# Kernel optimization log

Measured on AMD Instinct MI355X. Metric: run time of the kernel, lower is better.

The kernel has to match this reference:

```python
import jax, jax.numpy as jnp
import numpy as np

D = 512      # d_model
H = 8        # nhead
HD = D // H  # head dim
L = 8        # axis-0 length (torch seq dim, batch_first=False)
S = 128      # axis-1 length (torch batch dim; relation-tensor axis)
NL = 3       # encoder layers
EPS = 1e-5


def setup_inputs() -> dict:
    key = jax.random.key(0)
    ks = jax.random.split(key, 16)
    w = lambda k, shape: jax.random.normal(k, shape, jnp.float32) * 0.02
    return {
        "x": jax.random.normal(ks[0], (L, S, D), jnp.float32),
        # stacked per-layer transformer params (leading dim = NL)
        "attn_in_w": w(ks[1], (NL, 3 * D, D)), "attn_in_b": jnp.zeros((NL, 3 * D), jnp.float32),
        "attn_out_w": w(ks[2], (NL, D, D)),    "attn_out_b": jnp.zeros((NL, D), jnp.float32),
        "ln1_w": jnp.ones((NL, D), jnp.float32), "ln1_b": jnp.zeros((NL, D), jnp.float32),
        "ln2_w": jnp.ones((NL, D), jnp.float32), "ln2_b": jnp.zeros((NL, D), jnp.float32),
        "ff1_w": w(ks[3], (NL, 4 * D, D)), "ff1_b": jnp.zeros((NL, 4 * D), jnp.float32),
        "ff2_w": w(ks[4], (NL, D, 4 * D)), "ff2_b": jnp.zeros((NL, D), jnp.float32),
        "fln_w": jnp.ones((D,), jnp.float32), "fln_b": jnp.zeros((D,), jnp.float32),
        # 4 projection MLPs stacked: 0=sub, 1=obj, 2=verb_sub, 3=verb_obj
        "mlp_w0": w(ks[5], (4, D, D)), "mlp_b0": jnp.zeros((4, D), jnp.float32),
        "mlp_w1": w(ks[6], (4, D, D)), "mlp_b1": jnp.zeros((4, D), jnp.float32),
        "mlp_w2": w(ks[7], (4, D, D)), "mlp_b2": jnp.zeros((4, D), jnp.float32),
    }


def _ln(x, w, b):
    m = jnp.mean(x, axis=-1, keepdims=True)
    v = jnp.mean(jnp.square(x - m), axis=-1, keepdims=True)
    return (x - m) * jax.lax.rsqrt(v + EPS) * w + b


def _mha(x, in_w, in_b, out_w, out_b):
    # x: (L, B, D); attention over axis 0 (torch batch_first=False semantics)
    l, b, _ = x.shape
    qkv = x @ in_w.T + in_b                      # (L, B, 3D)
    q, k, v = jnp.split(qkv, 3, axis=-1)
    q = q.reshape(l, b, H, HD)
    k = k.reshape(l, b, H, HD)
    v = v.reshape(l, b, H, HD)
    scores = jnp.einsum("lbhd,mbhd->bhlm", q, k) / jnp.sqrt(jnp.float32(HD))
    attn = jax.nn.softmax(scores, axis=-1)
    o = jnp.einsum("bhlm,mbhd->lbhd", attn, v).reshape(l, b, D)
    return o @ out_w.T + out_b


def _mlp(x, w0, b0, w1, b1, w2, b2):
    h = jax.nn.relu(x @ w0.T + b0)
    h = jax.nn.relu(h @ w1.T + b1)
    return h @ w2.T + b2


def _forward(x, attn_in_w, attn_in_b, attn_out_w, attn_out_b,
             ln1_w, ln1_b, ln2_w, ln2_b, ff1_w, ff1_b, ff2_w, ff2_b,
             fln_w, fln_b, mlp_w0, mlp_b0, mlp_w1, mlp_b1, mlp_w2, mlp_b2):
    # TransformerEncoder (post-norm, relu, no dropout at eval)
    h = x
    for i in range(NL):
        h = _ln(h + _mha(h, attn_in_w[i], attn_in_b[i], attn_out_w[i], attn_out_b[i]),
                ln1_w[i], ln1_b[i])
        ff = jax.nn.relu(h @ ff1_w[i].T + ff1_b[i]) @ ff2_w[i].T + ff2_b[i]
        h = _ln(h + ff, ln2_w[i], ln2_b[i])
    h = _ln(h, fln_w, fln_b)  # final encoder norm

    sub = _mlp(h, mlp_w0[0], mlp_b0[0], mlp_w1[0], mlp_b1[0], mlp_w2[0], mlp_b2[0])
    obj = _mlp(h, mlp_w0[1], mlp_b0[1], mlp_w1[1], mlp_b1[1], mlp_w2[1], mlp_b2[1])
    vsub = _mlp(h, mlp_w0[2], mlp_b0[2], mlp_w1[2], mlp_b1[2], mlp_w2[2], mlp_b2[2])
    vobj = _mlp(h, mlp_w0[3], mlp_b0[3], mlp_w1[3], mlp_b1[3], mlp_w2[3], mlp_b2[3])

    # sub.unsqueeze(1) * vsub.unsqueeze(2): (B0, S, S, D)
    sub4 = sub[:, None, :, :] * vsub[:, :, None, :]
    obj4 = obj[:, None, :, :] * vobj[:, :, None, :]
    # p_x = sub4 @ obj4.transpose(-2, -1): (B0, S, S, S)
    return jnp.einsum("bijd,bikd->bijk", sub4, obj4)


def reference(x, attn_in_w, attn_in_b, attn_out_w, attn_out_b,
              ln1_w, ln1_b, ln2_w, ln2_b, ff1_w, ff1_b, ff2_w, ff2_b,
              fln_w, fln_b, mlp_w0, mlp_b0, mlp_w1, mlp_b1, mlp_w2, mlp_b2):
    return _forward(x, attn_in_w, attn_in_b, attn_out_w, attn_out_b,
                    ln1_w, ln1_b, ln2_w, ln2_b, ff1_w, ff1_b, ff2_w, ff2_b,
                    fln_w, fln_b, mlp_w0, mlp_b0, mlp_w1, mlp_b1, mlp_w2, mlp_b2)
```

## Files before the change

### kernel.cpp

```cpp
#include <hip/hip_runtime.h>

#define DEV __device__ __forceinline__

typedef __attribute__((ext_vector_type(8))) short bf16x8;
typedef __attribute__((ext_vector_type(8))) unsigned short u16x8;
typedef __attribute__((ext_vector_type(4))) float f32x4;

DEV unsigned short f2bf(float f) {
  unsigned int u = __float_as_uint(f);
  u += 0x7FFFu + ((u >> 16) & 1u);
  return (unsigned short)(u >> 16);
}
DEV float bf2f(unsigned short h) { return __uint_as_float(((unsigned int)h) << 16); }

DEV int swz(int row, int byteoff) { return row * 128 + (byteoff ^ ((row & 7) << 4)); }

__global__ void cvt_kernel(const float* __restrict__ src, unsigned short* __restrict__ dst,
                           float* __restrict__ dstf, int n) {
  long i = ((long)blockIdx.x * blockDim.x + threadIdx.x) * 8;
  long stride = (long)gridDim.x * blockDim.x * 8;
  for (; i < n; i += stride) {
    f32x4 a = *(const f32x4*)(src + i);
    f32x4 b = *(const f32x4*)(src + i + 4);
    u16x8 o;
    o[0] = f2bf(a[0]); o[1] = f2bf(a[1]); o[2] = f2bf(a[2]); o[3] = f2bf(a[3]);
    o[4] = f2bf(b[0]); o[5] = f2bf(b[1]); o[6] = f2bf(b[2]); o[7] = f2bf(b[3]);
    *(u16x8*)(dst + i) = o;
    if (dstf) { *(f32x4*)(dstf + i) = a; *(f32x4*)(dstf + i + 4) = b; }
  }
}

template <int ACT, int WF32, int WBF>
__global__ __launch_bounds__(256) void gemm_kernel(
    const unsigned short* __restrict__ X, const unsigned short* __restrict__ Wt,
    const float* __restrict__ bias, float* Yf, unsigned short* Ybf,
    int M, int N, int K, long xbs, long wbs, long bbs, long ybs) {
  __shared__ __align__(16) unsigned short As[64 * 64];
  __shared__ __align__(16) unsigned short Bs[64 * 64];
  const int t = threadIdx.x;
  const int bn = blockIdx.x, bm = blockIdx.y, bz = blockIdx.z;
  const unsigned short* Xp = X + (long)bz * xbs;
  const unsigned short* Wp = Wt + (long)bz * wbs;
  const float* bp = bias + (long)bz * bbs;

  const int lane = t & 63, wv = t >> 6;
  const int wr = wv >> 1, wc = wv & 1;
  f32x4 acc[2][2] = {};

  const int r = t >> 2;
  const int q = t & 3;
  const long xrow = (long)(bm * 64 + r) * K;
  const long wrow = (long)(bn * 64 + r) * K;
  char* Asb = (char*)As;
  char* Bsb = (char*)Bs;

  for (int kt = 0; kt < K; kt += 64) {
    const unsigned short* ga = Xp + xrow + kt + q * 16;
    const unsigned short* gb = Wp + wrow + kt + q * 16;
    u16x8 a0 = *(const u16x8*)ga;
    u16x8 a1 = *(const u16x8*)(ga + 8);
    u16x8 b0 = *(const u16x8*)gb;
    u16x8 b1 = *(const u16x8*)(gb + 8);
    *(u16x8*)(Asb + swz(r, q * 32)) = a0;
    *(u16x8*)(Asb + swz(r, q * 32 + 16)) = a1;
    *(u16x8*)(Bsb + swz(r, q * 32)) = b0;
    *(u16x8*)(Bsb + swz(r, q * 32 + 16)) = b1;
    __syncthreads();
#pragma unroll
    for (int kk = 0; kk < 2; ++kk) {
      const int kb = kk * 64 + ((lane >> 4) << 4);
      bf16x8 af[2], bfr[2];
#pragma unroll
      for (int mi = 0; mi < 2; ++mi)
        af[mi] = *(const bf16x8*)(Asb + swz(wr * 32 + mi * 16 + (lane & 15), kb));
#pragma unroll
      for (int ni = 0; ni < 2; ++ni)
        bfr[ni] = *(const bf16x8*)(Bsb + swz(wc * 32 + ni * 16 + (lane & 15), kb));
#pragma unroll
      for (int mi = 0; mi < 2; ++mi)
#pragma unroll
        for (int ni = 0; ni < 2; ++ni)
          acc[mi][ni] = __builtin_amdgcn_mfma_f32_16x16x32_bf16(af[mi], bfr[ni], acc[mi][ni], 0, 0, 0);
    }
    __syncthreads();
  }
#pragma unroll
  for (int ni = 0; ni < 2; ++ni) {
    const int n = bn * 64 + wc * 32 + ni * 16 + (lane & 15);
    const float bv = bp[n];
#pragma unroll
    for (int mi = 0; mi < 2; ++mi) {
#pragma unroll
      for (int rr = 0; rr < 4; ++rr) {
        const int gm = bm * 64 + wr * 32 + mi * 16 + ((lane >> 4) << 2) + rr;
        float v = acc[mi][ni][rr] + bv;
        if (ACT == 1) v = fmaxf(v, 0.f);
        const long o = (long)bz * ybs + (long)gm * N + n;
        if (WF32) Yf[o] = v;
        if (WBF) Ybf[o] = f2bf(v);
      }
    }
  }
}

__global__ __launch_bounds__(256) void attn_kernel(const unsigned short* __restrict__ qkv,
                                                   unsigned short* __restrict__ o) {
  __shared__ float P[512];
  const int s = blockIdx.x;
  const int t = threadIdx.x;
#pragma unroll
  for (int rep = 0; rep < 2; ++rep) {
    const int idx = t + rep * 256;
    const int h = idx >> 6, l = (idx >> 3) & 7, m = idx & 7;
    const unsigned short* qp = qkv + (long)(l * 128 + s) * 1536 + h * 64;
    const unsigned short* kp = qkv + (long)(m * 128 + s) * 1536 + 512 + h * 64;
    float acc = 0.f;
#pragma unroll
    for (int c = 0; c < 64; c += 8) {
      u16x8 q8 = *(const u16x8*)(qp + c);
      u16x8 k8 = *(const u16x8*)(kp + c);
#pragma unroll
      for (int j = 0; j < 8; ++j) acc += bf2f(q8[j]) * bf2f(k8[j]);
    }
    P[idx] = acc * 0.125f;
  }
  __syncthreads();
  if (t < 64) {
    const int base = t * 8;
    float mx = -1e30f;
#pragma unroll
    for (int m = 0; m < 8; ++m) mx = fmaxf(mx, P[base + m]);
    float e[8], sum = 0.f;
#pragma unroll
    for (int m = 0; m < 8; ++m) { e[m] = expf(P[base + m] - mx); sum += e[m]; }
    const float inv = 1.f / sum;
#pragma unroll
    for (int m = 0; m < 8; ++m) P[base + m] = e[m] * inv;
  }
  __syncthreads();
#pragma unroll
  for (int rep = 0; rep < 16; ++rep) {
    const int idx = t + rep * 256;
    const int d = idx & 63, h = (idx >> 6) & 7, l = idx >> 9;
    float acc = 0.f;
#pragma unroll
    for (int m = 0; m < 8; ++m)
      acc += P[h * 64 + l * 8 + m] * bf2f(qkv[(long)(m * 128 + s) * 1536 + 1024 + h * 64 + d]);
    o[(long)(l * 128 + s) * 512 + h * 64 + d] = f2bf(acc);
  }
}

template <int RES, int WF32>
__global__ __launch_bounds__(256) void ln_kernel(const float* a, const float* res,
                                                 const float* __restrict__ w,
                                                 const float* __restrict__ bb, float* hf,
                                                 unsigned short* __restrict__ hbf) {
  __shared__ float red[8];
  const int row = blockIdx.x, t = threadIdx.x;
  const long base = (long)row * 512;
  float x0 = a[base + t], x1 = a[base + t + 256];
  if (RES) { x0 += res[base + t]; x1 += res[base + t + 256]; }
  float s = x0 + x1;
#pragma unroll
  for (int msk = 32; msk; msk >>= 1) s += __shfl_xor(s, msk, 64);
  if ((t & 63) == 0) red[t >> 6] = s;
  __syncthreads();
  const float mean = (red[0] + red[1] + red[2] + red[3]) * (1.f / 512.f);
  const float d0 = x0 - mean, d1 = x1 - mean;
  float v = d0 * d0 + d1 * d1;
#pragma unroll
  for (int msk = 32; msk; msk >>= 1) v += __shfl_xor(v, msk, 64);
  if ((t & 63) == 0) red[4 + (t >> 6)] = v;
  __syncthreads();
  const float var = (red[4] + red[5] + red[6] + red[7]) * (1.f / 512.f);
  const float inv = rsqrtf(var + 1e-5f);
  const float o0 = d0 * inv * w[t] + bb[t];
  const float o1 = d1 * inv * w[t + 256] + bb[t + 256];
  if (WF32) { hf[base + t] = o0; hf[base + t + 256] = o1; }
  hbf[base + t] = f2bf(o0);
  hbf[base + t + 256] = f2bf(o1);
}

__global__ __launch_bounds__(256) void phasec_kernel(const float* __restrict__ subp,
                                                     const unsigned short* __restrict__ objbf,
                                                     const float* __restrict__ vsub,
                                                     const float* __restrict__ vobj,
                                                     float* __restrict__ out) {
  __shared__ __align__(16) unsigned short As[128 * 64];
  __shared__ __align__(16) unsigned short Bs[128 * 64];
  __shared__ float Wl[512];
  const int t = threadIdx.x;
  const int i = blockIdx.x, b = blockIdx.y;
  const long base_bi = ((long)b * 128 + i) * 512;
  for (int d = t; d < 512; d += 256) Wl[d] = vsub[base_bi + d] * vobj[base_bi + d];
  __syncthreads();

  const int lane = t & 63, wv = t >> 6;
  const int wr = wv >> 1, wc = wv & 1;
  f32x4 acc[4][4] = {};
  char* Asb = (char*)As;
  char* Bsb = (char*)Bs;

  const int sr = t >> 1;
  const int sh = t & 1;
  const long grow = ((long)b * 128 + sr) * 512;

  for (int kt = 0; kt < 512; kt += 64) {
#pragma unroll
    for (int g = 0; g < 4; ++g) {
      const int c = sh * 32 + g * 8;
      const float* gp = subp + grow + kt + c;
      f32x4 a = *(const f32x4*)gp;
      f32x4 b4 = *(const f32x4*)(gp + 4);
      const float* wp = Wl + kt + c;
      u16x8 oa;
      oa[0] = f2bf(a[0] * wp[0]); oa[1] = f2bf(a[1] * wp[1]);
      oa[2] = f2bf(a[2] * wp[2]); oa[3] = f2bf(a[3] * wp[3]);
      oa[4] = f2bf(b4[0] * wp[4]); oa[5] = f2bf(b4[1] * wp[5]);
      oa[6] = f2bf(b4[2] * wp[6]); oa[7] = f2bf(b4[3] * wp[7]);
      *(u16x8*)(Asb + swz(sr, sh * 64 + g * 16)) = oa;
      *(u16x8*)(Bsb + swz(sr, sh * 64 + g * 16)) = *(const u16x8*)(objbf + grow + kt + c);
    }
    __syncthreads();
#pragma unroll
    for (int kk = 0; kk < 2; ++kk) {
      const int kb = kk * 64 + ((lane >> 4) << 4);
      bf16x8 af[4], bfr[4];
#pragma unroll
      for (int mi = 0; mi < 4; ++mi)
        af[mi] = *(const bf16x8*)(Asb + swz(wr * 64 + mi * 16 + (lane & 15), kb));
#pragma unroll
      for (int ni = 0; ni < 4; ++ni)
        bfr[ni] = *(const bf16x8*)(Bsb + swz(wc * 64 + ni * 16 + (lane & 15), kb));
#pragma unroll
      for (int mi = 0; mi < 4; ++mi)
#pragma unroll
        for (int ni = 0; ni < 4; ++ni)
          acc[mi][ni] = __builtin_amdgcn_mfma_f32_16x16x32_bf16(af[mi], bfr[ni], acc[mi][ni], 0, 0, 0);
    }
    __syncthreads();
  }
  float* ob = out + ((long)b * 128 + i) * 128 * 128;
#pragma unroll
  for (int mi = 0; mi < 4; ++mi) {
#pragma unroll
    for (int rr = 0; rr < 4; ++rr) {
      const int j = wr * 64 + mi * 16 + ((lane >> 4) << 2) + rr;
      float* orow = ob + (long)j * 128 + wc * 64 + (lane & 15);
#pragma unroll
      for (int ni = 0; ni < 4; ++ni) orow[ni * 16] = acc[mi][ni][rr];
    }
  }
}

extern "C" void kernel_launch(void* const* d_in, const int* in_sizes, int n_in, void* d_out,
                              int out_size, void* d_ws, size_t ws_size, hipStream_t stream) {
  const float* x          = (const float*)d_in[0];
  const float* attn_in_w  = (const float*)d_in[1];
  const float* attn_in_b  = (const float*)d_in[2];
  const float* attn_out_w = (const float*)d_in[3];
  const float* attn_out_b = (const float*)d_in[4];
  const float* ln1_w = (const float*)d_in[5];
  const float* ln1_b = (const float*)d_in[6];
  const float* ln2_w = (const float*)d_in[7];
  const float* ln2_b = (const float*)d_in[8];
  const float* ff1_w = (const float*)d_in[9];
  const float* ff1_b = (const float*)d_in[10];
  const float* ff2_w = (const float*)d_in[11];
  const float* ff2_b = (const float*)d_in[12];
  const float* fln_w = (const float*)d_in[13];
  const float* fln_b = (const float*)d_in[14];
  const float* mlp_w0 = (const float*)d_in[15];
  const float* mlp_b0 = (const float*)d_in[16];
  const float* mlp_w1 = (const float*)d_in[17];
  const float* mlp_b1 = (const float*)d_in[18];
  const float* mlp_w2 = (const float*)d_in[19];
  const float* mlp_b2 = (const float*)d_in[20];
  float* out = (float*)d_out;
  (void)in_sizes; (void)n_in; (void)out_size; (void)ws_size;

  char* ws = (char*)d_ws;
  size_t off = 0;
  auto alloc = [&](size_t bytes) -> void* {
    void* p = (void*)(ws + off);
    off += (bytes + 255) & ~(size_t)255;
    return p;
  };
  unsigned short* wq  = (unsigned short*)alloc((size_t)3 * 1536 * 512 * 2);
  unsigned short* wo  = (unsigned short*)alloc((size_t)3 * 512 * 512 * 2);
  unsigned short* wf1 = (unsigned short*)alloc((size_t)3 * 2048 * 512 * 2);
  unsigned short* wf2 = (unsigned short*)alloc((size_t)3 * 512 * 2048 * 2);
  unsigned short* wm0 = (unsigned short*)alloc((size_t)4 * 512 * 512 * 2);
  unsigned short* wm1 = (unsigned short*)alloc((size_t)4 * 512 * 512 * 2);
  unsigned short* wm2 = (unsigned short*)alloc((size_t)4 * 512 * 512 * 2);
  float* h            = (float*)alloc((size_t)1024 * 512 * 4);
  unsigned short* hbf = (unsigned short*)alloc((size_t)1024 * 512 * 2);
  unsigned short* t1  = (unsigned short*)alloc((size_t)1024 * 2048 * 2);
  float* t2           = (float*)alloc((size_t)1024 * 512 * 4);
  unsigned short* ao  = (unsigned short*)alloc((size_t)1024 * 512 * 2);
  unsigned short* z1  = (unsigned short*)alloc((size_t)4 * 1024 * 512 * 2);
  unsigned short* z2  = (unsigned short*)alloc((size_t)4 * 1024 * 512 * 2);
  float* hf4          = (float*)alloc((size_t)4 * 1024 * 512 * 4);
  unsigned short* hb4 = (unsigned short*)alloc((size_t)4 * 1024 * 512 * 2);

  auto cvt = [&](const float* s, unsigned short* d, float* df, int n) {
    int blocks = (n / 8 + 255) / 256;
    cvt_kernel<<<blocks, 256, 0, stream>>>(s, d, df, n);
  };
  cvt(attn_in_w, wq, nullptr, 3 * 1536 * 512);
  cvt(attn_out_w, wo, nullptr, 3 * 512 * 512);
  cvt(ff1_w, wf1, nullptr, 3 * 2048 * 512);
  cvt(ff2_w, wf2, nullptr, 3 * 512 * 2048);
  cvt(mlp_w0, wm0, nullptr, 4 * 512 * 512);
  cvt(mlp_w1, wm1, nullptr, 4 * 512 * 512);
  cvt(mlp_w2, wm2, nullptr, 4 * 512 * 512);
  cvt(x, hbf, h, 1024 * 512);

  for (int i = 0; i < 3; ++i) {
    gemm_kernel<0, 0, 1><<<dim3(24, 16, 1), 256, 0, stream>>>(
        hbf, wq + (long)i * 1536 * 512, attn_in_b + i * 1536, nullptr, t1, 1024, 1536, 512, 0, 0, 0, 0);
    attn_kernel<<<128, 256, 0, stream>>>(t1, ao);
    gemm_kernel<0, 1, 0><<<dim3(8, 16, 1), 256, 0, stream>>>(
        ao, wo + (long)i * 512 * 512, attn_out_b + i * 512, t2, nullptr, 1024, 512, 512, 0, 0, 0, 0);
    ln_kernel<1, 1><<<1024, 256, 0, stream>>>(t2, h, ln1_w + i * 512, ln1_b + i * 512, h, hbf);
    gemm_kernel<1, 0, 1><<<dim3(32, 16, 1), 256, 0, stream>>>(
        hbf, wf1 + (long)i * 2048 * 512, ff1_b + i * 2048, nullptr, t1, 1024, 2048, 512, 0, 0, 0, 0);
    gemm_kernel<0, 1, 0><<<dim3(8, 16, 1), 256, 0, stream>>>(
        t1, wf2 + (long)i * 512 * 2048, ff2_b + i * 512, t2, nullptr, 1024, 512, 2048, 0, 0, 0, 0);
    ln_kernel<1, 1><<<1024, 256, 0, stream>>>(t2, h, ln2_w + i * 512, ln2_b + i * 512, h, hbf);
  }
  ln_kernel<0, 0><<<1024, 256, 0, stream>>>(h, nullptr, fln_w, fln_b, h, hbf);

  gemm_kernel<1, 0, 1><<<dim3(8, 16, 4), 256, 0, stream>>>(
      hbf, wm0, mlp_b0, nullptr, z1, 1024, 512, 512, 0, 512 * 512, 512, 1024 * 512);
  gemm_kernel<1, 0, 1><<<dim3(8, 16, 4), 256, 0, stream>>>(
      z1, wm1, mlp_b1, nullptr, z2, 1024, 512, 512, 1024 * 512, 512 * 512, 512, 1024 * 512);
  gemm_kernel<0, 1, 1><<<dim3(8, 16, 4), 256, 0, stream>>>(
      z2, wm2, mlp_b2, hf4, hb4, 1024, 512, 512, 1024 * 512, 512 * 512, 512, 1024 * 512);

  phasec_kernel<<<dim3(128, 8), 256, 0, stream>>>(
      hf4, hb4 + 1 * 1024 * 512, hf4 + 2L * 1024 * 512, hf4 + 3L * 1024 * 512, out);
}
```

Measured before the change: 450.4 us.

## Double-buffer GEMM and phase-C LDS tiles, add BM template, batch weight conversions

The GEMM and phase-C kernels now double-buffer their LDS tiles and prefetch the next K tile into registers, so global loads overlap MFMA work and only one barrier is needed per iteration. The GEMM gains a BM template parameter, and the N=512 GEMMs use 32-row tiles to launch twice as many blocks. The seven weight-conversion launches are merged into one multi-segment kernel, and f2bf now uses the HIP bf16 intrinsic. LDS use doubles, which can lower occupancy, and the extra prefetch registers add pressure.

```diff
diff --git a/kernel.cpp b/kernel.cpp
--- a/kernel.cpp
+++ b/kernel.cpp
@@ -1,4 +1,5 @@
 #include <hip/hip_runtime.h>
+#include <hip/hip_bf16.h>
 
 #define DEV __device__ __forceinline__
 
@@ -7,9 +8,7 @@
 typedef __attribute__((ext_vector_type(4))) float f32x4;
 
 DEV unsigned short f2bf(float f) {
-  unsigned int u = __float_as_uint(f);
-  u += 0x7FFFu + ((u >> 16) & 1u);
-  return (unsigned short)(u >> 16);
+  return __builtin_bit_cast(unsigned short, __float2bfloat16(f));
 }
 DEV float bf2f(unsigned short h) { return __uint_as_float(((unsigned int)h) << 16); }
 
@@ -30,69 +29,104 @@
   }
 }
 
-template <int ACT, int WF32, int WBF>
+struct CvtJobs { const float* s[7]; unsigned short* d[7]; int n[7]; };
+__global__ void cvtw_kernel(CvtJobs J) {
+  const int seg = blockIdx.y;
+  const float* __restrict__ src = J.s[seg];
+  unsigned short* __restrict__ dst = J.d[seg];
+  const int n = J.n[seg];
+  long i = ((long)blockIdx.x * blockDim.x + threadIdx.x) * 8;
+  long stride = (long)gridDim.x * blockDim.x * 8;
+  for (; i < n; i += stride) {
+    f32x4 a = *(const f32x4*)(src + i);
+    f32x4 b = *(const f32x4*)(src + i + 4);
+    u16x8 o;
+    o[0] = f2bf(a[0]); o[1] = f2bf(a[1]); o[2] = f2bf(a[2]); o[3] = f2bf(a[3]);
+    o[4] = f2bf(b[0]); o[5] = f2bf(b[1]); o[6] = f2bf(b[2]); o[7] = f2bf(b[3]);
+    *(u16x8*)(dst + i) = o;
+  }
+}
+
+template <int BM, int ACT, int WF32, int WBF>
 __global__ __launch_bounds__(256) void gemm_kernel(
     const unsigned short* __restrict__ X, const unsigned short* __restrict__ Wt,
-    const float* __restrict__ bias, float* Yf, unsigned short* Ybf,
+    const float* __restrict__ bias, float* Yf, unsigned short* __restrict__ Ybf,
     int M, int N, int K, long xbs, long wbs, long bbs, long ybs) {
-  __shared__ __align__(16) unsigned short As[64 * 64];
-  __shared__ __align__(16) unsigned short Bs[64 * 64];
+  constexpr int CA = (BM * 64) / (256 * 8);
+  constexpr int ABY = BM * 64 * 2;
+  constexpr int BBY = 64 * 64 * 2;
+  constexpr int MI = BM / 32;
+  __shared__ __align__(16) char Asb[2 * ABY];
+  __shared__ __align__(16) char Bsb[2 * BBY];
   const int t = threadIdx.x;
   const int bn = blockIdx.x, bm = blockIdx.y, bz = blockIdx.z;
   const unsigned short* Xp = X + (long)bz * xbs;
   const unsigned short* Wp = Wt + (long)bz * wbs;
-  const float* bp = bias + (long)bz * bbs;
 
   const int lane = t & 63, wv = t >> 6;
   const int wr = wv >> 1, wc = wv & 1;
-  f32x4 acc[2][2] = {};
-
-  const int r = t >> 2;
-  const int q = t & 3;
-  const long xrow = (long)(bm * 64 + r) * K;
-  const long wrow = (long)(bn * 64 + r) * K;
-  char* Asb = (char*)As;
-  char* Bsb = (char*)Bs;
-
-  for (int kt = 0; kt < K; kt += 64) {
-    const unsigned short* ga = Xp + xrow + kt + q * 16;
-    const unsigned short* gb = Wp + wrow + kt + q * 16;
-    u16x8 a0 = *(const u16x8*)ga;
-    u16x8 a1 = *(const u16x8*)(ga + 8);
-    u16x8 b0 = *(const u16x8*)gb;
-    u16x8 b1 = *(const u16x8*)(gb + 8);
-    *(u16x8*)(Asb + swz(r, q * 32)) = a0;
-    *(u16x8*)(Asb + swz(r, q * 32 + 16)) = a1;
-    *(u16x8*)(Bsb + swz(r, q * 32)) = b0;
-    *(u16x8*)(Bsb + swz(r, q * 32 + 16)) = b1;
-    __syncthreads();
+  f32x4 acc[MI][2] = {};
+
+  int rowA[CA], slotA[CA], rowB[2], slotB[2];
+#pragma unroll
+  for (int c = 0; c < CA; ++c) { int id = c * 256 + t; rowA[c] = id >> 3; slotA[c] = id & 7; }
+#pragma unroll
+  for (int c = 0; c < 2; ++c) { int id = c * 256 + t; rowB[c] = id >> 3; slotB[c] = id & 7; }
+
+  u16x8 ra[CA], rb[2];
+  auto load = [&](int kt) {
+#pragma unroll
+    for (int c = 0; c < CA; ++c)
+      ra[c] = *(const u16x8*)(Xp + (long)(bm * BM + rowA[c]) * K + kt + slotA[c] * 8);
+#pragma unroll
+    for (int c = 0; c < 2; ++c)
+      rb[c] = *(const u16x8*)(Wp + (long)(bn * 64 + rowB[c]) * K + kt + slotB[c] * 8);
+  };
+  auto store = [&](int cur) {
+#pragma unroll
+    for (int c = 0; c < CA; ++c)
+      *(u16x8*)(Asb + cur * ABY + swz(rowA[c], slotA[c] * 16)) = ra[c];
+#pragma unroll
+    for (int c = 0; c < 2; ++c)
+      *(u16x8*)(Bsb + cur * BBY + swz(rowB[c], slotB[c] * 16)) = rb[c];
+  };
+
+  const int NT = K >> 6;
+  load(0);
+  store(0);
+  load(64);
+  __syncthreads();
+  for (int ki = 0; ki < NT; ++ki) {
+    const int cur = ki & 1;
+    if (ki + 1 < NT) store(cur ^ 1);
+    if (ki + 2 < NT) load((ki + 2) << 6);
 #pragma unroll
     for (int kk = 0; kk < 2; ++kk) {
       const int kb = kk * 64 + ((lane >> 4) << 4);
-      bf16x8 af[2], bfr[2];
-#pragma unroll
-      for (int mi = 0; mi < 2; ++mi)
-        af[mi] = *(const bf16x8*)(Asb + swz(wr * 32 + mi * 16 + (lane & 15), kb));
+      bf16x8 af[MI], bfv[2];
+#pragma unroll
+      for (int mi = 0; mi < MI; ++mi)
+        af[mi] = *(const bf16x8*)(Asb + cur * ABY + swz(wr * (MI * 16) + mi * 16 + (lane & 15), kb));
 #pragma unroll
       for (int ni = 0; ni < 2; ++ni)
-        bfr[ni] = *(const bf16x8*)(Bsb + swz(wc * 32 + ni * 16 + (lane & 15), kb));
-#pragma unroll
-      for (int mi = 0; mi < 2; ++mi)
+        bfv[ni] = *(const bf16x8*)(Bsb + cur * BBY + swz(wc * 32 + ni * 16 + (lane & 15), kb));
+#pragma unroll
+      for (int mi = 0; mi < MI; ++mi)
 #pragma unroll
         for (int ni = 0; ni < 2; ++ni)
-          acc[mi][ni] = __builtin_amdgcn_mfma_f32_16x16x32_bf16(af[mi], bfr[ni], acc[mi][ni], 0, 0, 0);
+          acc[mi][ni] = __builtin_amdgcn_mfma_f32_16x16x32_bf16(af[mi], bfv[ni], acc[mi][ni], 0, 0, 0);
     }
     __syncthreads();
   }
 #pragma unroll
   for (int ni = 0; ni < 2; ++ni) {
     const int n = bn * 64 + wc * 32 + ni * 16 + (lane & 15);
-    const float bv = bp[n];
-#pragma unroll
-    for (int mi = 0; mi < 2; ++mi) {
+    const float bv = bias[(long)bz * bbs + n];
+#pragma unroll
+    for (int mi = 0; mi < MI; ++mi) {
 #pragma unroll
       for (int rr = 0; rr < 4; ++rr) {
-        const int gm = bm * 64 + wr * 32 + mi * 16 + ((lane >> 4) << 2) + rr;
+        const int gm = bm * BM + wr * (MI * 16) + mi * 16 + ((lane >> 4) << 2) + rr;
         float v = acc[mi][ni][rr] + bv;
         if (ACT == 1) v = fmaxf(v, 0.f);
         const long o = (long)bz * ybs + (long)gm * N + n;
@@ -186,57 +220,74 @@
                                                      const float* __restrict__ vsub,
                                                      const float* __restrict__ vobj,
                                                      float* __restrict__ out) {
-  __shared__ __align__(16) unsigned short As[128 * 64];
-  __shared__ __align__(16) unsigned short Bs[128 * 64];
+  constexpr int ABY = 128 * 64 * 2;
+  __shared__ __align__(16) char Asb[2 * ABY];
+  __shared__ __align__(16) char Bsb[2 * ABY];
   __shared__ float Wl[512];
   const int t = threadIdx.x;
   const int i = blockIdx.x, b = blockIdx.y;
   const long base_bi = ((long)b * 128 + i) * 512;
   for (int d = t; d < 512; d += 256) Wl[d] = vsub[base_bi + d] * vobj[base_bi + d];
-  __syncthreads();
 
   const int lane = t & 63, wv = t >> 6;
   const int wr = wv >> 1, wc = wv & 1;
   f32x4 acc[4][4] = {};
-  char* Asb = (char*)As;
-  char* Bsb = (char*)Bs;
-
-  const int sr = t >> 1;
-  const int sh = t & 1;
-  const long grow = ((long)b * 128 + sr) * 512;
-
-  for (int kt = 0; kt < 512; kt += 64) {
-#pragma unroll
-    for (int g = 0; g < 4; ++g) {
-      const int c = sh * 32 + g * 8;
-      const float* gp = subp + grow + kt + c;
-      f32x4 a = *(const f32x4*)gp;
-      f32x4 b4 = *(const f32x4*)(gp + 4);
-      const float* wp = Wl + kt + c;
+
+  int row[4], slot[4];
+#pragma unroll
+  for (int c = 0; c < 4; ++c) { int id = c * 256 + t; row[c] = id >> 3; slot[c] = id & 7; }
+
+  f32x4 fa[4][2];
+  u16x8 rb[4];
+  auto load = [&](int kt) {
+#pragma unroll
+    for (int c = 0; c < 4; ++c) {
+      const long g = ((long)b * 128 + row[c]) * 512 + kt + slot[c] * 8;
+      fa[c][0] = *(const f32x4*)(subp + g);
+      fa[c][1] = *(const f32x4*)(subp + g + 4);
+      rb[c] = *(const u16x8*)(objbf + g);
+    }
+  };
+  auto store = [&](int cur, int ktd) {
+#pragma unroll
+    for (int c = 0; c < 4; ++c) {
+      const float* wp = Wl + ktd + slot[c] * 8;
+      f32x4 w0 = *(const f32x4*)wp;
+      f32x4 w1 = *(const f32x4*)(wp + 4);
       u16x8 oa;
-      oa[0] = f2bf(a[0] * wp[0]); oa[1] = f2bf(a[1] * wp[1]);
-      oa[2] = f2bf(a[2] * wp[2]); oa[3] = f2bf(a[3] * wp[3]);
-      oa[4] = f2bf(b4[0] * wp[4]); oa[5] = f2bf(b4[1] * wp[5]);
-      oa[6] = f2bf(b4[2] * wp[6]); oa[7] = f2bf(b4[3] * wp[7]);
-      *(u16x8*)(Asb + swz(sr, sh * 64 + g * 16)) = oa;
-      *(u16x8*)(Bsb + swz(sr, sh * 64 + g * 16)) = *(const u16x8*)(objbf + grow + kt + c);
-    }
-    __syncthreads();
+      oa[0] = f2bf(fa[c][0][0] * w0[0]); oa[1] = f2bf(fa[c][0][1] * w0[1]);
+      oa[2] = f2bf(fa[c][0][2] * w0[2]); oa[3] = f2bf(fa[c][0][3] * w0[3]);
+      oa[4] = f2bf(fa[c][1][0] * w1[0]); oa[5] = f2bf(fa[c][1][1] * w1[1]);
+      oa[6] = f2bf(fa[c][1][2] * w1[2]); oa[7] = f2bf(fa[c][1][3] * w1[3]);
+      *(u16x8*)(Asb + cur * ABY + swz(row[c], slot[c] * 16)) = oa;
+      *(u16x8*)(Bsb + cur * ABY + swz(row[c], slot[c] * 16)) = rb[c];
+    }
+  };
+
+  __syncthreads();
+  load(0);
+  store(0, 0);
+  load(64);
+  __syncthreads();
+  for (int ki = 0; ki < 8; ++ki) {
+    const int cur = ki & 1;
+    if (ki + 1 < 8) store(cur ^ 1, (ki + 1) * 64);
+    if (ki + 2 < 8) load((ki + 2) * 64);
 #pragma unroll
     for (int kk = 0; kk < 2; ++kk) {
       const int kb = kk * 64 + ((lane >> 4) << 4);
-      bf16x8 af[4], bfr[4];
+      bf16x8 af[4], bfv[4];
 #pragma unroll
       for (int mi = 0; mi < 4; ++mi)
-        af[mi] = *(const bf16x8*)(Asb + swz(wr * 64 + mi * 16 + (lane & 15), kb));
+        af[mi] = *(const bf16x8*)(Asb + cur * ABY + swz(wr * 64 + mi * 16 + (lane & 15), kb));
 #pragma unroll
       for (int ni = 0; ni < 4; ++ni)
-        bfr[ni] = *(const bf16x8*)(Bsb + swz(wc * 64 + ni * 16 + (lane & 15), kb));
+        bfv[ni] = *(const bf16x8*)(Bsb + cur * ABY + swz(wc * 64 + ni * 16 + (lane & 15), kb));
 #pragma unroll
       for (int mi = 0; mi < 4; ++mi)
 #pragma unroll
         for (int ni = 0; ni < 4; ++ni)
-          acc[mi][ni] = __builtin_amdgcn_mfma_f32_16x16x32_bf16(af[mi], bfr[ni], acc[mi][ni], 0, 0, 0);
+          acc[mi][ni] = __builtin_amdgcn_mfma_f32_16x16x32_bf16(af[mi], bfv[ni], acc[mi][ni], 0, 0, 0);
     }
     __syncthreads();
   }
@@ -303,39 +354,37 @@
   float* hf4          = (float*)alloc((size_t)4 * 1024 * 512 * 4);
   unsigned short* hb4 = (unsigned short*)alloc((size_t)4 * 1024 * 512 * 2);
 
-  auto cvt = [&](const float* s, unsigned short* d, float* df, int n) {
-    int blocks = (n / 8 + 255) / 256;
-    cvt_kernel<<<blocks, 256, 0, stream>>>(s, d, df, n);
-  };
-  cvt(attn_in_w, wq, nullptr, 3 * 1536 * 512);
-  cvt(attn_out_w, wo, nullptr, 3 * 512 * 512);
-  cvt(ff1_w, wf1, nullptr, 3 * 2048 * 512);
-  cvt(ff2_w, wf2, nullptr, 3 * 512 * 2048);
-  cvt(mlp_w0, wm0, nullptr, 4 * 512 * 512);
-  cvt(mlp_w1, wm1, nullptr, 4 * 512 * 512);
-  cvt(mlp_w2, wm2, nullptr, 4 * 512 * 512);
-  cvt(x, hbf, h, 1024 * 512);
+  CvtJobs J;
+  J.s[0] = attn_in_w;  J.d[0] = wq;  J.n[0] = 3 * 1536 * 512;
+  J.s[1] = attn_out_w; J.d[1] = wo;  J.n[1] = 3 * 512 * 512;
+  J.s[2] = ff1_w;      J.d[2] = wf1; J.n[2] = 3 * 2048 * 512;
+  J.s[3] = ff2_w;      J.d[3] = wf2; J.n[3] = 3 * 512 * 2048;
+  J.s[4] = mlp_w0;     J.d[4] = wm0; J.n[4] = 4 * 512 * 512;
+  J.s[5] = mlp_w1;     J.d[5] = wm1; J.n[5] = 4 * 512 * 512;
+  J.s[6] = mlp_w2;     J.d[6] = wm2; J.n[6] = 4 * 512 * 512;
+  cvtw_kernel<<<dim3(512, 7), 256, 0, stream>>>(J);
+  cvt_kernel<<<256, 256, 0, stream>>>(x, hbf, h, 1024 * 512);
 
   for (int i = 0; i < 3; ++i) {
-    gemm_kernel<0, 0, 1><<<dim3(24, 16, 1), 256, 0, stream>>>(
+    gemm_kernel<64, 0, 0, 1><<<dim3(24, 16, 1), 256, 0, stream>>>(
         hbf, wq + (long)i * 1536 * 512, attn_in_b + i * 1536, nullptr, t1, 1024, 1536, 512, 0, 0, 0, 0);
     attn_kernel<<<128, 256, 0, stream>>>(t1, ao);
-    gemm_kernel<0, 1, 0><<<dim3(8, 16, 1), 256, 0, stream>>>(
+    gemm_kernel<32, 0, 1, 0><<<dim3(8, 32, 1), 256, 0, stream>>>(
         ao, wo + (long)i * 512 * 512, attn_out_b + i * 512, t2, nullptr, 1024, 512, 512, 0, 0, 0, 0);
     ln_kernel<1, 1><<<1024, 256, 0, stream>>>(t2, h, ln1_w + i * 512, ln1_b + i * 512, h, hbf);
-    gemm_kernel<1, 0, 1><<<dim3(32, 16, 1), 256, 0, stream>>>(
+    gemm_kernel<64, 1, 0, 1><<<dim3(32, 16, 1), 256, 0, stream>>>(
         hbf, wf1 + (long)i * 2048 * 512, ff1_b + i * 2048, nullptr, t1, 1024, 2048, 512, 0, 0, 0, 0);
-    gemm_kernel<0, 1, 0><<<dim3(8, 16, 1), 256, 0, stream>>>(
+    gemm_kernel<32, 0, 1, 0><<<dim3(8, 32, 1), 256, 0, stream>>>(
         t1, wf2 + (long)i * 512 * 2048, ff2_b + i * 512, t2, nullptr, 1024, 512, 2048, 0, 0, 0, 0);
     ln_kernel<1, 1><<<1024, 256, 0, stream>>>(t2, h, ln2_w + i * 512, ln2_b + i * 512, h, hbf);
   }
   ln_kernel<0, 0><<<1024, 256, 0, stream>>>(h, nullptr, fln_w, fln_b, h, hbf);
 
-  gemm_kernel<1, 0, 1><<<dim3(8, 16, 4), 256, 0, stream>>>(
+  gemm_kernel<32, 1, 0, 1><<<dim3(8, 32, 4), 256, 0, stream>>>(
       hbf, wm0, mlp_b0, nullptr, z1, 1024, 512, 512, 0, 512 * 512, 512, 1024 * 512);
-  gemm_kernel<1, 0, 1><<<dim3(8, 16, 4), 256, 0, stream>>>(
+  gemm_kernel<32, 1, 0, 1><<<dim3(8, 32, 4), 256, 0, stream>>>(
       z1, wm1, mlp_b1, nullptr, z2, 1024, 512, 512, 1024 * 512, 512 * 512, 512, 1024 * 512);
-  gemm_kernel<0, 1, 1><<<dim3(8, 16, 4), 256, 0, stream>>>(
+  gemm_kernel<32, 0, 1, 1><<<dim3(8, 32, 4), 256, 0, stream>>>(
       z2, wm2, mlp_b2, hf4, hb4, 1024, 512, 512, 1024 * 512, 512 * 512, 512, 1024 * 512);
 
   phasec_kernel<<<dim3(128, 8), 256, 0, stream>>>(
```

Measured after the change: 379.6 us. 1.19x faster.
